# Kernel optimization log

Hardware: AMD Instinct MI355X
Metric: run time of the kernel (lower is better)

Reference implementation:

```python
import jax, jax.numpy as jnp
import numpy as np

B, T, D_IN, D_OUT, R = 4, 4096, 2048, 2048, 64
SCALING = 2.0  # alpha / r = 128 / 64


def setup_inputs() -> dict:
    key = jax.random.key(0)
    k_x, k_w, k_a, k_b = jax.random.split(key, 4)
    x = jax.random.normal(k_x, (B, T, D_IN), dtype=jnp.float32)
    weight = jax.random.normal(k_w, (D_OUT, D_IN), dtype=jnp.float32) * 0.02
    lora_A = jax.random.normal(k_a, (R, D_IN), dtype=jnp.float32) * 0.02
    lora_B = jax.random.normal(k_b, (D_OUT, R), dtype=jnp.float32) * 0.02
    return {"x": x, "weight": weight, "lora_A": lora_A, "lora_B": lora_B}


def reference(x, weight, lora_A, lora_B):
    # Base (dequantized) linear: F.linear(x, W) with W [out, in]
    base = jnp.einsum("btd,od->bto", x, weight)
    # LoRA low-rank correction: scaling * (x @ A^T) @ B^T
    lora = jnp.einsum("btr,or->bto", jnp.einsum("btd,rd->btr", x, lora_A), lora_B)
    return base + SCALING * lora
```

## Files before the change

### kernel.cpp

```cpp
#include <hip/hip_runtime.h>
#include <hip/hip_bf16.h>


typedef short short8 __attribute__((ext_vector_type(8)));
typedef float f32x4 __attribute__((ext_vector_type(4)));

#define TK 32
#define SLOT_BYTES 32768

__device__ __forceinline__ unsigned short f2bf(float f) {
  unsigned u = __float_as_uint(f);
  u += 0x7fff + ((u >> 16) & 1);
  return (unsigned short)(u >> 16);
}

__global__ __launch_bounds__(256) void cvt_x_kernel(const float* __restrict__ x,
                                                    unsigned short* __restrict__ xb,
                                                    long long n) {
  long long idx = ((long long)blockIdx.x * 256 + threadIdx.x) * 8;
  long long stride = (long long)gridDim.x * 256 * 8;
  for (; idx < n; idx += stride) {
    float4 v0 = *(const float4*)(x + idx);
    float4 v1 = *(const float4*)(x + idx + 4);
    short8 o;
    o[0] = (short)f2bf(v0.x); o[1] = (short)f2bf(v0.y);
    o[2] = (short)f2bf(v0.z); o[3] = (short)f2bf(v0.w);
    o[4] = (short)f2bf(v1.x); o[5] = (short)f2bf(v1.y);
    o[6] = (short)f2bf(v1.z); o[7] = (short)f2bf(v1.w);
    *(short8*)(xb + idx) = o;
  }
}

__global__ __launch_bounds__(256) void weff_kernel(const float* __restrict__ W,
                                                   const float* __restrict__ Alora,
                                                   const float* __restrict__ Blora,
                                                   unsigned short* __restrict__ Weff,
                                                   int N, int K, int R, float scaling) {
  __shared__ float Bs[16][64];
  int t = threadIdx.x;
  int ob = blockIdx.y * 16;
  int i = blockIdx.x * 256 + t;
  for (int j = t; j < 16 * 64; j += 256)
    Bs[j >> 6][j & 63] = Blora[(ob + (j >> 6)) * R + (j & 63)];
  __syncthreads();
  float acc[16];
#pragma unroll
  for (int o = 0; o < 16; ++o) acc[o] = 0.f;
#pragma unroll 8
  for (int r = 0; r < 64; ++r) {
    float av = Alora[r * K + i];
#pragma unroll
    for (int o = 0; o < 16; ++o) acc[o] = fmaf(Bs[o][r], av, acc[o]);
  }
#pragma unroll
  for (int o = 0; o < 16; ++o) {
    float w = W[(size_t)(ob + o) * K + i];
    Weff[(size_t)(ob + o) * K + i] = f2bf(w + scaling * acc[o]);
  }
}

#define GLOAD_LDS16(g, l)                                                        \
  __builtin_amdgcn_global_load_lds((const __attribute__((address_space(1))) void*)(g), \
                                   (__attribute__((address_space(3))) void*)(l), 16, 0, 0)


__global__ __launch_bounds__(512, 2) void gemm256_kernel(const unsigned short* __restrict__ Xb,
                                                         const unsigned short* __restrict__ Wb,
                                                         float* __restrict__ out,
                                                         int M, int N, int K) {
  __shared__ __align__(16) char lds[4 * SLOT_BYTES];

  const int t = threadIdx.x;
  const int lane = t & 63;
  const int w = t >> 6;
  const int wr = w >> 2, wc = w & 3;

  const int nwg = gridDim.x;
  const int cpx = nwg >> 3;
  const int swz = (blockIdx.x & 7) * cpx + (blockIdx.x >> 3);
  const int nbn = N >> 8;
  const int bm = swz / nbn, bn = swz % nbn;

  f32x4 acc[8][4];
  const f32x4 z = {0.f, 0.f, 0.f, 0.f};
#pragma unroll
  for (int i = 0; i < 8; ++i)
#pragma unroll
    for (int j = 0; j < 4; ++j) acc[i][j] = z;

  const int vs = (t >> 3) & 7;
  const int p0 = (t * 16) ^ (vs << 4);
  const int sm = p0 >> 6;
  const int sk = ((p0 >> 4) & 3) * 8;
  const unsigned short* gA0 = Xb + (size_t)(bm * 256 + sm) * K + sk;
  const unsigned short* gB0 = Wb + (size_t)(bn * 256 + sm) * K + sk;

#define STAGE(SLOT, KOFF)                                                   \
  { char* la_ = lds + (SLOT) * SLOT_BYTES;                                  \
    GLOAD_LDS16(gA0 + (KOFF),                   la_ + t * 16);              \
    GLOAD_LDS16(gA0 + (size_t)128 * K + (KOFF), la_ + 8192 + t * 16);       \
    GLOAD_LDS16(gB0 + (KOFF),                   la_ + 16384 + t * 16);      \
    GLOAD_LDS16(gB0 + (size_t)128 * K + (KOFF), la_ + 24576 + t * 16); }

  const int lane15 = lane & 15, ksl = lane >> 4;
  const int vr = (lane15 >> 1) & 7;
  const int abase = (((wr * 128 + lane15) * 64) + ksl * 16) ^ (vr << 4);
  const int bbase = 16384 + (((((wc * 64) + lane15) * 64) + ksl * 16) ^ (vr << 4));

#define PHASE_BODY(SLOT)                                                    \
  { char* lp_ = lds + (SLOT) * SLOT_BYTES;                                  \
    short8 af[8], bfr[4];                                                   \
    _Pragma("unroll") for (int i = 0; i < 8; ++i)                           \
      af[i] = *(const short8*)(lp_ + abase + i * 1024);                     \
    _Pragma("unroll") for (int j = 0; j < 4; ++j)                           \
      bfr[j] = *(const short8*)(lp_ + bbase + j * 1024);                    \
    __builtin_amdgcn_s_setprio(1);                                          \
    _Pragma("unroll") for (int i = 0; i < 8; ++i)                           \
      _Pragma("unroll") for (int j = 0; j < 4; ++j)                         \
        acc[i][j] = __builtin_amdgcn_mfma_f32_16x16x32_bf16(af[i], bfr[j],  \
                                                            acc[i][j], 0, 0, 0); \
    __builtin_amdgcn_s_setprio(0); }

#define WAITBAR(NSTR)                                                       \
  asm volatile("s_waitcnt vmcnt(" NSTR ")" ::: "memory");                   \
  __builtin_amdgcn_s_barrier();                                             \
  __builtin_amdgcn_sched_barrier(0);

  const int NT = K / TK;
  STAGE(0, 0)
  STAGE(1, TK)
  STAGE(2, 2 * TK)

  for (int u = 0; u < NT - 3; ++u) {
    WAITBAR("8")
    STAGE((u + 3) & 3, (u + 3) * TK)
    PHASE_BODY(u & 3)
  }
  WAITBAR("8") PHASE_BODY((NT - 3) & 3)
  WAITBAR("4") PHASE_BODY((NT - 2) & 3)
  WAITBAR("0") PHASE_BODY((NT - 1) & 3)

  const int orow0 = bm * 256 + wr * 128 + ksl * 4;
  const int ocol0 = bn * 256 + wc * 64 + lane15;
#pragma unroll
  for (int i = 0; i < 8; ++i)
#pragma unroll
    for (int j = 0; j < 4; ++j) {
      size_t base = (size_t)(orow0 + i * 16) * N + (ocol0 + j * 16);
#pragma unroll
      for (int q = 0; q < 4; ++q) out[base + (size_t)q * N] = acc[i][j][q];
    }
}

extern "C" void kernel_launch(void* const* d_in, const int* in_sizes, int n_in,
                              void* d_out, int out_size, void* d_ws, size_t ws_size,
                              hipStream_t stream) {
  const float* x  = (const float*)d_in[0];
  const float* W  = (const float*)d_in[1];
  const float* Al = (const float*)d_in[2];
  const float* Bl = (const float*)d_in[3];
  float* out = (float*)d_out;

  const int K = 2048;
  const long long M = (long long)in_sizes[0] / K;
  const int N = in_sizes[1] / K;
  const int R = in_sizes[2] / K;

  unsigned short* xb   = (unsigned short*)d_ws;
  unsigned short* weff = xb + (size_t)M * K;

  cvt_x_kernel<<<2048, 256, 0, stream>>>(x, xb, (long long)M * K);
  weff_kernel<<<dim3(K / 256, N / 16), 256, 0, stream>>>(W, Al, Bl, weff, N, K, R, 2.0f);
  gemm256_kernel<<<(N / 256) * (int)(M / 256), 512, 0, stream>>>(xb, weff, out, (int)M, N, K);
}
```

Measured before the change: 395.9 us.

## Double-buffer LDS fragment registers to overlap LDS reads with MFMA

Splits the per-tile phase into separate fragment-read and MFMA steps and keeps two register fragment sets. The LDS reads for the next k-tile are issued before the MFMAs on the current fragments, with the loop unrolled by two. The goal is to hide LDS read latency behind matrix-core work. In exchange it doubles fragment register usage (48 extra VGPRs), which could cause spills under launch_bounds(512,2). The prologue, steady-state loop and epilogue were all re-sequenced to keep slot reuse consistent with the 4-slot ring.

```diff
diff --git a/kernel.cpp b/kernel.cpp
--- a/kernel.cpp
+++ b/kernel.cpp
@@ -63,7 +63,6 @@
   __builtin_amdgcn_global_load_lds((const __attribute__((address_space(1))) void*)(g), \
                                    (__attribute__((address_space(3))) void*)(l), 16, 0, 0)
 
-
 __global__ __launch_bounds__(512, 2) void gemm256_kernel(const unsigned short* __restrict__ Xb,
                                                          const unsigned short* __restrict__ Wb,
                                                          float* __restrict__ out,
@@ -107,38 +106,62 @@
   const int abase = (((wr * 128 + lane15) * 64) + ksl * 16) ^ (vr << 4);
   const int bbase = 16384 + (((((wc * 64) + lane15) * 64) + ksl * 16) ^ (vr << 4));
 
-#define PHASE_BODY(SLOT)                                                    \
+#define READ_FRAGS(AF, BF, SLOT)                                            \
   { char* lp_ = lds + (SLOT) * SLOT_BYTES;                                  \
-    short8 af[8], bfr[4];                                                   \
     _Pragma("unroll") for (int i = 0; i < 8; ++i)                           \
-      af[i] = *(const short8*)(lp_ + abase + i * 1024);                     \
+      AF[i] = *(const short8*)(lp_ + abase + i * 1024);                     \
     _Pragma("unroll") for (int j = 0; j < 4; ++j)                           \
-      bfr[j] = *(const short8*)(lp_ + bbase + j * 1024);                    \
-    __builtin_amdgcn_s_setprio(1);                                          \
-    _Pragma("unroll") for (int i = 0; i < 8; ++i)                           \
-      _Pragma("unroll") for (int j = 0; j < 4; ++j)                         \
-        acc[i][j] = __builtin_amdgcn_mfma_f32_16x16x32_bf16(af[i], bfr[j],  \
-                                                            acc[i][j], 0, 0, 0); \
-    __builtin_amdgcn_s_setprio(0); }
+      BF[j] = *(const short8*)(lp_ + bbase + j * 1024); }
 
-#define WAITBAR(NSTR)                                                       \
-  asm volatile("s_waitcnt vmcnt(" NSTR ")" ::: "memory");                   \
+#define MFMA_SET(AF, BF)                                                    \
+  __builtin_amdgcn_s_setprio(1);                                            \
+  _Pragma("unroll") for (int i = 0; i < 8; ++i)                             \
+    _Pragma("unroll") for (int j = 0; j < 4; ++j)                           \
+      acc[i][j] = __builtin_amdgcn_mfma_f32_16x16x32_bf16(AF[i], BF[j],     \
+                                                          acc[i][j], 0, 0, 0); \
+  __builtin_amdgcn_s_setprio(0);
+
+#define WAITBAR2(VM)                                                        \
+  asm volatile("s_waitcnt vmcnt(" VM ") lgkmcnt(0)" ::: "memory");          \
   __builtin_amdgcn_s_barrier();                                             \
   __builtin_amdgcn_sched_barrier(0);
 
+  short8 afA[8], bfA[4], afB[8], bfB[4];
+
   const int NT = K / TK;
+
   STAGE(0, 0)
   STAGE(1, TK)
   STAGE(2, 2 * TK)
+  WAITBAR2("8")
+  READ_FRAGS(afA, bfA, 0)
+  STAGE(3, 3 * TK)
 
-  for (int u = 0; u < NT - 3; ++u) {
-    WAITBAR("8")
+  for (int u = 1; u <= NT - 4; u += 2) {
+    WAITBAR2("8")
     STAGE((u + 3) & 3, (u + 3) * TK)
-    PHASE_BODY(u & 3)
+    READ_FRAGS(afB, bfB, u & 3)
+    MFMA_SET(afA, bfA)
+
+    WAITBAR2("8")
+    STAGE((u + 4) & 3, (u + 4) * TK)
+    READ_FRAGS(afA, bfA, (u + 1) & 3)
+    MFMA_SET(afB, bfB)
   }
-  WAITBAR("8") PHASE_BODY((NT - 3) & 3)
-  WAITBAR("4") PHASE_BODY((NT - 2) & 3)
-  WAITBAR("0") PHASE_BODY((NT - 1) & 3)
+
+  WAITBAR2("8")
+  READ_FRAGS(afB, bfB, (NT - 3) & 3)
+  MFMA_SET(afA, bfA)
+
+  WAITBAR2("4")
+  READ_FRAGS(afA, bfA, (NT - 2) & 3)
+  MFMA_SET(afB, bfB)
+
+  WAITBAR2("0")
+  READ_FRAGS(afB, bfB, (NT - 1) & 3)
+  MFMA_SET(afA, bfA)
+
+  MFMA_SET(afB, bfB)
 
   const int orow0 = bm * 256 + wr * 128 + ksl * 4;
   const int ocol0 = bn * 256 + wc * 64 + lane15;
```

Result: no change. 389.6 us (-1.6%).

## Restructure GEMM main loop into 8-phase ping-pong schedule with 64-wide K tiles

Applied to the files above, without the earlier changes.

Replaces the 4-slot, 32-wide K pipeline with a two-buffer scheme of 64-wide K tiles, each split into four phases. Each phase reads half the A fragments and issues part of the next tile's global-to-LDS loads before a barrier and a block of MFMAs. The aim is to interleave LDS reads, async global loads and MFMA work at finer grain and to lower register pressure by holding only 4 A fragments at a time. It adds many more barriers per K step and uses a new swizzle, and the loop count is hardcoded for K=2048.

```diff
diff --git a/kernel.cpp b/kernel.cpp
--- a/kernel.cpp
+++ b/kernel.cpp
@@ -4,9 +4,6 @@
 
 typedef short short8 __attribute__((ext_vector_type(8)));
 typedef float f32x4 __attribute__((ext_vector_type(4)));
-
-#define TK 32
-#define SLOT_BYTES 32768
 
 __device__ __forceinline__ unsigned short f2bf(float f) {
   unsigned u = __float_as_uint(f);
@@ -64,19 +61,18 @@
                                    (__attribute__((address_space(3))) void*)(l), 16, 0, 0)
 
 
-__global__ __launch_bounds__(512, 2) void gemm256_kernel(const unsigned short* __restrict__ Xb,
-                                                         const unsigned short* __restrict__ Wb,
-                                                         float* __restrict__ out,
-                                                         int M, int N, int K) {
-  __shared__ __align__(16) char lds[4 * SLOT_BYTES];
+__global__ __launch_bounds__(512, 2) void gemm8p_kernel(const unsigned short* __restrict__ Xb,
+                                                        const unsigned short* __restrict__ Wb,
+                                                        float* __restrict__ out,
+                                                        int M, int N, int K) {
+  __shared__ __align__(16) char lds[131072];
 
   const int t = threadIdx.x;
   const int lane = t & 63;
   const int w = t >> 6;
   const int wr = w >> 2, wc = w & 3;
 
-  const int nwg = gridDim.x;
-  const int cpx = nwg >> 3;
+  const int nwg = gridDim.x, cpx = nwg >> 3;
   const int swz = (blockIdx.x & 7) * cpx + (blockIdx.x >> 3);
   const int nbn = N >> 8;
   const int bm = swz / nbn, bn = swz % nbn;
@@ -88,57 +84,87 @@
 #pragma unroll
     for (int j = 0; j < 4; ++j) acc[i][j] = z;
 
-  const int vs = (t >> 3) & 7;
-  const int p0 = (t * 16) ^ (vs << 4);
-  const int sm = p0 >> 6;
-  const int sk = ((p0 >> 4) & 3) * 8;
-  const unsigned short* gA0 = Xb + (size_t)(bm * 256 + sm) * K + sk;
-  const unsigned short* gB0 = Wb + (size_t)(bn * 256 + sm) * K + sk;
-
-#define STAGE(SLOT, KOFF)                                                   \
-  { char* la_ = lds + (SLOT) * SLOT_BYTES;                                  \
-    GLOAD_LDS16(gA0 + (KOFF),                   la_ + t * 16);              \
-    GLOAD_LDS16(gA0 + (size_t)128 * K + (KOFF), la_ + 8192 + t * 16);       \
-    GLOAD_LDS16(gB0 + (KOFF),                   la_ + 16384 + t * 16);      \
-    GLOAD_LDS16(gB0 + (size_t)128 * K + (KOFF), la_ + 24576 + t * 16); }
+  const int srow = (t >> 2) ^ ((t >> 5) & 1);
+  const int scol = ((t & 3) ^ ((t >> 3) & 3)) * 8;
+  const unsigned short* gA = Xb + (size_t)(bm * 256 + srow) * K + scol;
+  const unsigned short* gB = Wb + (size_t)(bn * 256 + srow) * K + scol;
 
   const int lane15 = lane & 15, ksl = lane >> 4;
-  const int vr = (lane15 >> 1) & 7;
-  const int abase = (((wr * 128 + lane15) * 64) + ksl * 16) ^ (vr << 4);
-  const int bbase = 16384 + (((((wc * 64) + lane15) * 64) + ksl * 16) ^ (vr << 4));
-
-#define PHASE_BODY(SLOT)                                                    \
-  { char* lp_ = lds + (SLOT) * SLOT_BYTES;                                  \
-    short8 af[8], bfr[4];                                                   \
-    _Pragma("unroll") for (int i = 0; i < 8; ++i)                           \
-      af[i] = *(const short8*)(lp_ + abase + i * 1024);                     \
-    _Pragma("unroll") for (int j = 0; j < 4; ++j)                           \
-      bfr[j] = *(const short8*)(lp_ + bbase + j * 1024);                    \
-    __builtin_amdgcn_s_setprio(1);                                          \
-    _Pragma("unroll") for (int i = 0; i < 8; ++i)                           \
-      _Pragma("unroll") for (int j = 0; j < 4; ++j)                         \
-        acc[i][j] = __builtin_amdgcn_mfma_f32_16x16x32_bf16(af[i], bfr[j],  \
-                                                            acc[i][j], 0, 0, 0); \
-    __builtin_amdgcn_s_setprio(0); }
-
-#define WAITBAR(NSTR)                                                       \
-  asm volatile("s_waitcnt vmcnt(" NSTR ")" ::: "memory");                   \
-  __builtin_amdgcn_s_barrier();                                             \
-  __builtin_amdgcn_sched_barrier(0);
-
-  const int NT = K / TK;
-  STAGE(0, 0)
-  STAGE(1, TK)
-  STAGE(2, 2 * TK)
-
-  for (int u = 0; u < NT - 3; ++u) {
-    WAITBAR("8")
-    STAGE((u + 3) & 3, (u + 3) * TK)
-    PHASE_BODY(u & 3)
-  }
-  WAITBAR("8") PHASE_BODY((NT - 3) & 3)
-  WAITBAR("4") PHASE_BODY((NT - 2) & 3)
-  WAITBAR("0") PHASE_BODY((NT - 1) & 3)
+  const int key = ((lane15 >> 1) & 7) << 4;
+  const int aRead = (((wr * 128 + lane15) * 64) + ksl * 16) ^ key;
+  const int bRead = (((wc * 64 + lane15) * 64) + ksl * 16) ^ key;
+
+  short8 af0, af1, af2, af3, bf0, bf1, bf2, bf3;
+
+#define STG_A(NS, KSU, KOFF)                                                    \
+  GLOAD_LDS16(gA + (KOFF), lds + (NS) * 65536 + (KSU) * 16384 + t * 16);        \
+  GLOAD_LDS16(gA + (size_t)128 * K + (KOFF),                                    \
+              lds + (NS) * 65536 + (KSU) * 16384 + 8192 + t * 16);
+#define STG_B(NS, KSU, KOFF)                                                    \
+  GLOAD_LDS16(gB + (KOFF), lds + (NS) * 65536 + 32768 + (KSU) * 16384 + t * 16);\
+  GLOAD_LDS16(gB + (size_t)128 * K + (KOFF),                                    \
+              lds + (NS) * 65536 + 32768 + (KSU) * 16384 + 8192 + t * 16);
+
+#define RD_A(SLOT, KSU, MB) {                                                   \
+    const char* p_ = lds + (SLOT) * 65536 + (KSU) * 16384 + aRead + (MB) * 1024;\
+    af0 = *(const short8*)(p_);                                                 \
+    af1 = *(const short8*)(p_ + 1024);                                          \
+    af2 = *(const short8*)(p_ + 2048);                                          \
+    af3 = *(const short8*)(p_ + 3072); }
+#define RD_B(SLOT, KSU) {                                                       \
+    const char* p_ = lds + (SLOT) * 65536 + 32768 + (KSU) * 16384 + bRead;      \
+    bf0 = *(const short8*)(p_);                                                 \
+    bf1 = *(const short8*)(p_ + 1024);                                          \
+    bf2 = *(const short8*)(p_ + 2048);                                          \
+    bf3 = *(const short8*)(p_ + 3072); }
+
+#define MM4(AF, MI)                                                             \
+  acc[MI][0] = __builtin_amdgcn_mfma_f32_16x16x32_bf16(AF, bf0, acc[MI][0], 0, 0, 0); \
+  acc[MI][1] = __builtin_amdgcn_mfma_f32_16x16x32_bf16(AF, bf1, acc[MI][1], 0, 0, 0); \
+  acc[MI][2] = __builtin_amdgcn_mfma_f32_16x16x32_bf16(AF, bf2, acc[MI][2], 0, 0, 0); \
+  acc[MI][3] = __builtin_amdgcn_mfma_f32_16x16x32_bf16(AF, bf3, acc[MI][3], 0, 0, 0);
+
+#define PH(SLOT, KSU, MB, RDB_STMT, STG_STMT, WAIT_STMT)                        \
+  RD_A(SLOT, KSU, MB)                                                           \
+  RDB_STMT                                                                      \
+  STG_STMT                                                                      \
+  WAIT_STMT                                                                     \
+  __builtin_amdgcn_s_barrier();                                                 \
+  asm volatile("s_waitcnt lgkmcnt(0)" ::: "memory");                            \
+  __builtin_amdgcn_sched_barrier(0);                                            \
+  __builtin_amdgcn_s_setprio(1);                                                \
+  MM4(af0, (MB) + 0) MM4(af1, (MB) + 1) MM4(af2, (MB) + 2) MM4(af3, (MB) + 3)   \
+  __builtin_amdgcn_s_setprio(0);                                                \
+  __builtin_amdgcn_s_barrier();
+
+#define VM4 asm volatile("s_waitcnt vmcnt(4)" ::: "memory");
+#define VM0 asm volatile("s_waitcnt vmcnt(0)" ::: "memory");
+#define NOP_
+
+#define KTILE(SLOT, NS, KNEXT)                                                  \
+  PH(SLOT, 0, 0, RD_B(SLOT, 0), STG_A(NS, 0, KNEXT), NOP_)                      \
+  PH(SLOT, 0, 4, NOP_,          STG_B(NS, 0, KNEXT), VM4)                       \
+  PH(SLOT, 1, 0, RD_B(SLOT, 1), STG_A(NS, 1, (KNEXT) + 32), NOP_)               \
+  PH(SLOT, 1, 4, NOP_,          STG_B(NS, 1, (KNEXT) + 32), VM4)
+
+#define KTILE_LAST(SLOT)                                                        \
+  PH(SLOT, 0, 0, RD_B(SLOT, 0), NOP_, NOP_)                                     \
+  PH(SLOT, 0, 4, NOP_,          NOP_, VM0)                                      \
+  PH(SLOT, 1, 0, RD_B(SLOT, 1), NOP_, NOP_)                                     \
+  PH(SLOT, 1, 4, NOP_,          NOP_, NOP_)
+
+  STG_A(0, 0, 0) STG_B(0, 0, 0) STG_A(0, 1, 32) STG_B(0, 1, 32)
+  VM4
+  __builtin_amdgcn_s_barrier();
+
+  int kk = 64;
+#pragma unroll 1
+  for (int it = 0; it < 15; ++it) {
+    KTILE(0, 1, kk) kk += 64;
+    KTILE(1, 0, kk) kk += 64;
+  }
+  KTILE(0, 1, kk)
+  KTILE_LAST(1)
 
   const int orow0 = bm * 256 + wr * 128 + ksl * 4;
   const int ocol0 = bn * 256 + wc * 64 + lane15;
@@ -171,5 +197,5 @@
 
   cvt_x_kernel<<<2048, 256, 0, stream>>>(x, xb, (long long)M * K);
   weff_kernel<<<dim3(K / 256, N / 16), 256, 0, stream>>>(W, Al, Bl, weff, N, K, R, 2.0f);
-  gemm256_kernel<<<(N / 256) * (int)(M / 256), 512, 0, stream>>>(xb, weff, out, (int)M, N, K);
-}
+  gemm8p_kernel<<<(N / 256) * (int)(M / 256), 512, 0, stream>>>(xb, weff, out, (int)M, N, K);
+}
```

New measurement: 389.1 us. About the same (-1.7%).
